# Optimization experiments

Hardware: AMD Instinct MI355X
Metric: run time of the kernel (lower is better)

The kernel has to match this reference:

```python
import jax, jax.numpy as jnp
import numpy as np

N_TOKENS = 32768
DIM = 2048
N_EXPERTS = 64
TOP_K = 8
N_GROUP = 8
TOPK_GROUP = 4
ROUTE_SCALE = 2.5
EPS = 1e-20


def setup_inputs() -> dict:
    key = jax.random.key(0)
    k1, k2 = jax.random.split(key)
    hidden_states = jax.random.normal(k1, (N_TOKENS, DIM), dtype=jnp.float32)
    weight = jax.random.normal(k2, (N_EXPERTS, DIM), dtype=jnp.float32) * 0.02
    e_score_correction_bias = jnp.zeros((N_EXPERTS,), dtype=jnp.float32)
    return {"hidden_states": hidden_states, "weight": weight,
            "e_score_correction_bias": e_score_correction_bias}


def reference(hidden_states, weight, e_score_correction_bias):
    # router logits in fp32: [N, E]
    logits = jnp.einsum('nd,ed->ne', hidden_states.astype(jnp.float32),
                        weight.astype(jnp.float32))
    scores = jax.nn.sigmoid(logits)  # score_func == 'sigmoid'

    # --- top-k index selection (no-grad path in torch) ---
    sfc = scores + e_score_correction_bias[None, :]  # [N, E]
    per_group = N_EXPERTS // N_GROUP
    # group score = sum of top-2 scores within each group: [N, G]
    grouped = sfc.reshape(-1, N_GROUP, per_group)
    group_scores = jax.lax.top_k(grouped, 2)[0].sum(axis=-1)
    # pick top `TOPK_GROUP` groups
    _, group_idx = jax.lax.top_k(group_scores, TOPK_GROUP)  # [N, topk_group]
    n = group_scores.shape[0]
    group_mask = jnp.zeros_like(group_scores).at[
        jnp.arange(n)[:, None], group_idx].set(1.0)  # [N, G]
    score_mask = jnp.repeat(group_mask, per_group, axis=1)  # [N, E]
    masked_scores = jnp.where(score_mask > 0, sfc, 0.0)
    _, topk_indices = jax.lax.top_k(masked_scores, TOP_K)  # [N, top_k]

    # gather weights from *unbiased* scores, normalize, scale
    topk_weights = jnp.take_along_axis(scores, topk_indices, axis=1)
    denom = topk_weights.sum(axis=-1, keepdims=True) + EPS
    topk_weights = topk_weights / denom * ROUTE_SCALE
    return topk_indices, topk_weights
```

## Files before the change

kernel.cpp:

```cpp
#include <hip/hip_runtime.h>
#include <math.h>

#define NT 32768
#define DIM 2048
#define NE 64
#define RSCALE 2.5f
#define REPS 1e-20f
#define KC 32
#define NCH (DIM / KC)
#define TOK 64

#define HL_BUF 12288
#define WL_OFF 24576
#define BS_OFF 49152
#define ARENA 49408

typedef __attribute__((ext_vector_type(8))) short short8x;
typedef __attribute__((ext_vector_type(4))) float f32x4;
typedef __attribute__((ext_vector_type(4))) unsigned int uint4x;

#define PACKHI(odd, even) __builtin_amdgcn_perm((odd), (even), 0x07060302u)

__device__ __forceinline__ void decomp4(f32x4 x, unsigned int o[6]) {
    unsigned int u0 = __float_as_uint(x.x), u1 = __float_as_uint(x.y);
    unsigned int u2 = __float_as_uint(x.z), u3 = __float_as_uint(x.w);
    o[0] = PACKHI(u1, u0); o[1] = PACKHI(u3, u2);
    float r0 = x.x - __uint_as_float(u0 & 0xffff0000u);
    float r1 = x.y - __uint_as_float(u1 & 0xffff0000u);
    float r2 = x.z - __uint_as_float(u2 & 0xffff0000u);
    float r3 = x.w - __uint_as_float(u3 & 0xffff0000u);
    unsigned int v0 = __float_as_uint(r0), v1 = __float_as_uint(r1);
    unsigned int v2 = __float_as_uint(r2), v3 = __float_as_uint(r3);
    o[2] = PACKHI(v1, v0); o[3] = PACKHI(v3, v2);
    float s0 = r0 - __uint_as_float(v0 & 0xffff0000u);
    float s1 = r1 - __uint_as_float(v1 & 0xffff0000u);
    float s2 = r2 - __uint_as_float(v2 & 0xffff0000u);
    float s3 = r3 - __uint_as_float(v3 & 0xffff0000u);
    o[4] = PACKHI(__float_as_uint(s1), __float_as_uint(s0));
    o[5] = PACKHI(__float_as_uint(s3), __float_as_uint(s2));
}

__device__ __forceinline__ void decomp8(f32x4 a, f32x4 b,
                                        short8x* f0, short8x* f1, short8x* f2) {
    unsigned int oa[6], ob[6];
    decomp4(a, oa); decomp4(b, ob);
    uint4x t0 = {oa[0], oa[1], ob[0], ob[1]};
    uint4x t1 = {oa[2], oa[3], ob[2], ob[3]};
    uint4x t2 = {oa[4], oa[5], ob[4], ob[5]};
    *f0 = __builtin_bit_cast(short8x, t0);
    *f1 = __builtin_bit_cast(short8x, t1);
    *f2 = __builtin_bit_cast(short8x, t2);
}

#define STAGE_ISSUE(SA, SB, KOFF) do { \
    SA = *(const f32x4*)(gsrc + (KOFF));     \
    SB = *(const f32x4*)(gsrc + (KOFF) + 4); \
} while (0)

#define STAGE_WRITE(SA, SB, PN) do { \
    short8x f0_, f1_, f2_; \
    decomp8(SA, SB, &f0_, &f1_, &f2_); \
    *(short8x*)(arena + sbase + (PN) * HL_BUF + 0 * 4096 + soff) = f0_; \
    *(short8x*)(arena + sbase + (PN) * HL_BUF + 1 * 4096 + soff) = f1_; \
    *(short8x*)(arena + sbase + (PN) * HL_BUF + 2 * 4096 + soff) = f2_; \
} while (0)

#define COMPUTE(P) do { \
    const char* hb = arena + (P) * HL_BUF; \
    const char* wb = arena + WL_OFF + (P) * HL_BUF; \
    short8x a0, a1, a2; \
    { const int t_ = tt * 16 + l15; \
      const int ro_ = t_ * 64 + ((g ^ ((t_ >> 1) & 3)) << 4); \
      a0 = *(const short8x*)(hb + 0 * 4096 + ro_); \
      a1 = *(const short8x*)(hb + 1 * 4096 + ro_); \
      a2 = *(const short8x*)(hb + 2 * 4096 + ro_); } \
    _Pragma("unroll") \
    for (int et = 0; et < 2; ++et) { \
        const int e_ = ep * 32 + et * 16 + l15; \
        const int ro_ = e_ * 64 + ((g ^ ((e_ >> 1) & 3)) << 4); \
        short8x b0 = *(const short8x*)(wb + 0 * 4096 + ro_); \
        short8x b1 = *(const short8x*)(wb + 1 * 4096 + ro_); \
        short8x b2 = *(const short8x*)(wb + 2 * 4096 + ro_); \
        Cm[et] = __builtin_amdgcn_mfma_f32_16x16x32_bf16(a0, b0, Cm[et], 0, 0, 0); \
        Cc[et] = __builtin_amdgcn_mfma_f32_16x16x32_bf16(a1, b0, Cc[et], 0, 0, 0); \
        Cc[et] = __builtin_amdgcn_mfma_f32_16x16x32_bf16(a2, b0, Cc[et], 0, 0, 0); \
        Cc[et] = __builtin_amdgcn_mfma_f32_16x16x32_bf16(a0, b1, Cc[et], 0, 0, 0); \
        Cc[et] = __builtin_amdgcn_mfma_f32_16x16x32_bf16(a1, b1, Cc[et], 0, 0, 0); \
        Cc[et] = __builtin_amdgcn_mfma_f32_16x16x32_bf16(a0, b2, Cc[et], 0, 0, 0); \
    } \
} while (0)

#define DRAIN do { \
    _Pragma("unroll") \
    for (int et = 0; et < 2; ++et) { \
        _Pragma("unroll") \
        for (int r = 0; r < 4; ++r) \
            md[et][r] += (double)Cm[et][r] + (double)Cc[et][r]; \
        Cm[et] = (f32x4)0.0f; Cc[et] = (f32x4)0.0f; \
    } \
} while (0)

__global__ __launch_bounds__(512, 4) void router_kernel(
    const float* __restrict__ H,
    const float* __restrict__ W,
    const float* __restrict__ B,
    float* __restrict__ out)
{
    __shared__ __align__(16) char arena[ARENA];
    float* bsf = (float*)(arena + BS_OFF);
    float* scf = (float*)(arena);

    const int tid  = threadIdx.x;
    const int lane = tid & 63;
    const int w    = __builtin_amdgcn_readfirstlane(tid >> 6);
    const int l15  = lane & 15, g = lane >> 4;
    const size_t tb = (size_t)blockIdx.x * TOK;

    if (tid < NE) bsf[tid] = B[tid];

    const int si   = tid & 255;
    const int srow = si >> 2;
    const int sq   = si & 3;
    const bool isH = tid < 256;
    const float* gsrc = isH ? (H + (tb + (size_t)srow) * DIM + sq * 8)
                            : (W + (size_t)srow * DIM + sq * 8);
    const int sbase = isH ? 0 : WL_OFF;
    const int soff  = srow * 64 + ((sq ^ ((srow >> 1) & 3)) << 4);

    const int tt = w & 3, ep = w >> 2;

    f32x4 Cm[2], Cc[2];
    double md[2][4];
    #pragma unroll
    for (int et = 0; et < 2; ++et) {
        Cm[et] = (f32x4)0.0f; Cc[et] = (f32x4)0.0f;
        #pragma unroll
        for (int r = 0; r < 4; ++r) md[et][r] = 0.0;
    }

    f32x4 sA0, sA1, sB0, sB1;

    STAGE_ISSUE(sA0, sA1, 0);
    STAGE_WRITE(sA0, sA1, 0);
    STAGE_ISSUE(sB0, sB1, KC);
    __syncthreads();

    for (int chb = 0; chb < NCH; chb += 2) {
        if (chb + 2 < NCH) STAGE_ISSUE(sA0, sA1, (chb + 2) * KC);
        COMPUTE(0);
        STAGE_WRITE(sB0, sB1, 1);
        __syncthreads();

        if (chb + 3 < NCH) STAGE_ISSUE(sB0, sB1, (chb + 3) * KC);
        COMPUTE(1);
        if (chb + 2 < NCH) STAGE_WRITE(sA0, sA1, 0);
        if (((chb + 1) & 7) == 7) DRAIN;
        __syncthreads();
    }

    #pragma unroll
    for (int et = 0; et < 2; ++et)
        #pragma unroll
        for (int r = 0; r < 4; ++r) {
            float logit = (float)md[et][r];
            float s = 1.0f / (1.0f + expf(-logit));
            int t = tt * 16 + g * 4 + r;
            int e = ep * 32 + et * 16 + l15;
            scf[t * 65 + e] = s;
        }
    __syncthreads();

    if ((tid & 7) == 0) {
        const int t = tid >> 3;
        const float* sc = &scf[t * 65];
        float gs[8];
        #pragma unroll
        for (int gg = 0; gg < 8; ++gg) {
            float m1 = -1e30f, m2 = -1e30f;
            #pragma unroll
            for (int j = 0; j < 8; ++j) {
                float v = sc[gg * 8 + j] + bsf[gg * 8 + j];
                if (v > m1) { m2 = m1; m1 = v; }
                else if (v > m2) { m2 = v; }
            }
            gs[gg] = m1 + m2;
        }
        unsigned gmask = 0;
        for (int i = 0; i < 4; ++i) {
            float best = -1e30f; int bg = 0;
            for (int gg = 0; gg < 8; ++gg)
                if (!((gmask >> gg) & 1u) && gs[gg] > best) { best = gs[gg]; bg = gg; }
            gmask |= 1u << bg;
        }
        unsigned long long picked = 0ull;
        int   idxs[8];
        float wts[8];
        float wsum = 0.0f;
        for (int i = 0; i < 8; ++i) {
            float best = -1e30f; int bi = 0;
            for (int e = 0; e < 64; ++e) {
                if ((picked >> e) & 1ull) continue;
                float v = ((gmask >> (e >> 3)) & 1u) ? (sc[e] + bsf[e]) : 0.0f;
                if (v > best) { best = v; bi = e; }
            }
            picked |= 1ull << bi;
            idxs[i] = bi;
            wts[i] = sc[bi];
            wsum += sc[bi];
        }
        const float scale = RSCALE / (wsum + REPS);
        const size_t token = tb + t;
        #pragma unroll
        for (int i = 0; i < 8; ++i) {
            out[token * 8 + i] = (float)idxs[i];
            out[(size_t)NT * 8 + token * 8 + i] = wts[i] * scale;
        }
    }
}

extern "C" void kernel_launch(void* const* d_in, const int* in_sizes, int n_in,
                              void* d_out, int out_size, void* d_ws, size_t ws_size,
                              hipStream_t stream) {
    (void)in_sizes; (void)n_in; (void)out_size; (void)d_ws; (void)ws_size;
    const float* H = (const float*)d_in[0];
    const float* W = (const float*)d_in[1];
    const float* B = (const float*)d_in[2];
    float* out = (float*)d_out;
    router_kernel<<<dim3(NT / TOK), dim3(512), 0, stream>>>(H, W, B, out);
}
```

Baseline: 142.0 us.

## Predecompose router weights once and stream activations directly into registers

A separate pre-kernel splits the weight matrix once into three bf16 parts, stored in a global array laid out in MFMA fragment order. The main kernel drops the LDS staging and the per-chunk barriers. Each wave loads its own 16 token rows straight from global memory into registers, splits them there, and computes all 64 experts with fragments read from global, which should mostly hit cache. Block size falls to 256 threads and occupancy to 2 blocks. This removes redundant per-block weight splitting and LDS traffic, but adds a second launch and relies on cache bandwidth for weight reads, with no LDS reuse.

After: 223.5 us. +57.4%, slower.

```diff
diff --git a/kernel.cpp b/kernel.cpp
--- a/kernel.cpp
+++ b/kernel.cpp
@@ -10,14 +10,11 @@
 #define NCH (DIM / KC)
 #define TOK 64
 
-#define HL_BUF 12288
-#define WL_OFF 24576
-#define BS_OFF 49152
-#define ARENA 49408
-
 typedef __attribute__((ext_vector_type(8))) short short8x;
 typedef __attribute__((ext_vector_type(4))) float f32x4;
 typedef __attribute__((ext_vector_type(4))) unsigned int uint4x;
+
+__device__ short8x WLf[3][NCH][4][64];
 
 #define PACKHI(odd, even) __builtin_amdgcn_perm((odd), (even), 0x07060302u)
 
@@ -52,63 +49,28 @@
     *f2 = __builtin_bit_cast(short8x, t2);
 }
 
-#define STAGE_ISSUE(SA, SB, KOFF) do { \
-    SA = *(const f32x4*)(gsrc + (KOFF));     \
-    SB = *(const f32x4*)(gsrc + (KOFF) + 4); \
-} while (0)
-
-#define STAGE_WRITE(SA, SB, PN) do { \
-    short8x f0_, f1_, f2_; \
-    decomp8(SA, SB, &f0_, &f1_, &f2_); \
-    *(short8x*)(arena + sbase + (PN) * HL_BUF + 0 * 4096 + soff) = f0_; \
-    *(short8x*)(arena + sbase + (PN) * HL_BUF + 1 * 4096 + soff) = f1_; \
-    *(short8x*)(arena + sbase + (PN) * HL_BUF + 2 * 4096 + soff) = f2_; \
-} while (0)
-
-#define COMPUTE(P) do { \
-    const char* hb = arena + (P) * HL_BUF; \
-    const char* wb = arena + WL_OFF + (P) * HL_BUF; \
-    short8x a0, a1, a2; \
-    { const int t_ = tt * 16 + l15; \
-      const int ro_ = t_ * 64 + ((g ^ ((t_ >> 1) & 3)) << 4); \
-      a0 = *(const short8x*)(hb + 0 * 4096 + ro_); \
-      a1 = *(const short8x*)(hb + 1 * 4096 + ro_); \
-      a2 = *(const short8x*)(hb + 2 * 4096 + ro_); } \
-    _Pragma("unroll") \
-    for (int et = 0; et < 2; ++et) { \
-        const int e_ = ep * 32 + et * 16 + l15; \
-        const int ro_ = e_ * 64 + ((g ^ ((e_ >> 1) & 3)) << 4); \
-        short8x b0 = *(const short8x*)(wb + 0 * 4096 + ro_); \
-        short8x b1 = *(const short8x*)(wb + 1 * 4096 + ro_); \
-        short8x b2 = *(const short8x*)(wb + 2 * 4096 + ro_); \
-        Cm[et] = __builtin_amdgcn_mfma_f32_16x16x32_bf16(a0, b0, Cm[et], 0, 0, 0); \
-        Cc[et] = __builtin_amdgcn_mfma_f32_16x16x32_bf16(a1, b0, Cc[et], 0, 0, 0); \
-        Cc[et] = __builtin_amdgcn_mfma_f32_16x16x32_bf16(a2, b0, Cc[et], 0, 0, 0); \
-        Cc[et] = __builtin_amdgcn_mfma_f32_16x16x32_bf16(a0, b1, Cc[et], 0, 0, 0); \
-        Cc[et] = __builtin_amdgcn_mfma_f32_16x16x32_bf16(a1, b1, Cc[et], 0, 0, 0); \
-        Cc[et] = __builtin_amdgcn_mfma_f32_16x16x32_bf16(a0, b2, Cc[et], 0, 0, 0); \
-    } \
-} while (0)
-
-#define DRAIN do { \
-    _Pragma("unroll") \
-    for (int et = 0; et < 2; ++et) { \
-        _Pragma("unroll") \
-        for (int r = 0; r < 4; ++r) \
-            md[et][r] += (double)Cm[et][r] + (double)Cc[et][r]; \
-        Cm[et] = (f32x4)0.0f; Cc[et] = (f32x4)0.0f; \
-    } \
-} while (0)
-
-__global__ __launch_bounds__(512, 4) void router_kernel(
+__global__ void decomp_w_kernel(const float* __restrict__ W) {
+    const int ch = blockIdx.x;
+    const int et = threadIdx.x >> 6;
+    const int l  = threadIdx.x & 63;
+    const float* src = W + (size_t)(et * 16 + (l & 15)) * DIM + ch * KC + (l >> 4) * 8;
+    f32x4 lo = *(const f32x4*)src;
+    f32x4 hi = *(const f32x4*)(src + 4);
+    short8x f0, f1, f2;
+    decomp8(lo, hi, &f0, &f1, &f2);
+    WLf[0][ch][et][l] = f0;
+    WLf[1][ch][et][l] = f1;
+    WLf[2][ch][et][l] = f2;
+}
+
+__global__ __launch_bounds__(256, 2) void router_kernel(
     const float* __restrict__ H,
     const float* __restrict__ W,
     const float* __restrict__ B,
     float* __restrict__ out)
 {
-    __shared__ __align__(16) char arena[ARENA];
-    float* bsf = (float*)(arena + BS_OFF);
-    float* scf = (float*)(arena);
+    __shared__ float scf[TOK * 65];
+    __shared__ float bsf[NE];
 
     const int tid  = threadIdx.x;
     const int lane = tid & 63;
@@ -118,60 +80,69 @@
 
     if (tid < NE) bsf[tid] = B[tid];
 
-    const int si   = tid & 255;
-    const int srow = si >> 2;
-    const int sq   = si & 3;
-    const bool isH = tid < 256;
-    const float* gsrc = isH ? (H + (tb + (size_t)srow) * DIM + sq * 8)
-                            : (W + (size_t)srow * DIM + sq * 8);
-    const int sbase = isH ? 0 : WL_OFF;
-    const int soff  = srow * 64 + ((sq ^ ((srow >> 1) & 3)) << 4);
-
-    const int tt = w & 3, ep = w >> 2;
-
-    f32x4 Cm[2], Cc[2];
-    double md[2][4];
+    const float* hsrc = H + (tb + (size_t)(w * 16 + l15)) * DIM + g * 8;
+
+    f32x4 Cm[4], Cc[4];
+    double md[4][4];
     #pragma unroll
-    for (int et = 0; et < 2; ++et) {
+    for (int et = 0; et < 4; ++et) {
         Cm[et] = (f32x4)0.0f; Cc[et] = (f32x4)0.0f;
         #pragma unroll
         for (int r = 0; r < 4; ++r) md[et][r] = 0.0;
     }
 
-    f32x4 sA0, sA1, sB0, sB1;
-
-    STAGE_ISSUE(sA0, sA1, 0);
-    STAGE_WRITE(sA0, sA1, 0);
-    STAGE_ISSUE(sB0, sB1, KC);
-    __syncthreads();
-
-    for (int chb = 0; chb < NCH; chb += 2) {
-        if (chb + 2 < NCH) STAGE_ISSUE(sA0, sA1, (chb + 2) * KC);
-        COMPUTE(0);
-        STAGE_WRITE(sB0, sB1, 1);
-        __syncthreads();
-
-        if (chb + 3 < NCH) STAGE_ISSUE(sB0, sB1, (chb + 3) * KC);
-        COMPUTE(1);
-        if (chb + 2 < NCH) STAGE_WRITE(sA0, sA1, 0);
-        if (((chb + 1) & 7) == 7) DRAIN;
-        __syncthreads();
+    f32x4 aLo = *(const f32x4*)hsrc;
+    f32x4 aHi = *(const f32x4*)(hsrc + 4);
+
+    #pragma unroll 2
+    for (int ch = 0; ch < NCH; ++ch) {
+        const int chn = (ch + 1 < NCH) ? (ch + 1) : ch;
+        const float* np = hsrc + chn * KC;
+        f32x4 nLo = *(const f32x4*)np;
+        f32x4 nHi = *(const f32x4*)(np + 4);
+
+        short8x a0, a1, a2;
+        decomp8(aLo, aHi, &a0, &a1, &a2);
+
+        #pragma unroll
+        for (int et = 0; et < 4; ++et) {
+            short8x b0 = WLf[0][ch][et][lane];
+            short8x b1 = WLf[1][ch][et][lane];
+            short8x b2 = WLf[2][ch][et][lane];
+            Cm[et] = __builtin_amdgcn_mfma_f32_16x16x32_bf16(a0, b0, Cm[et], 0, 0, 0);
+            Cc[et] = __builtin_amdgcn_mfma_f32_16x16x32_bf16(a1, b0, Cc[et], 0, 0, 0);
+            Cc[et] = __builtin_amdgcn_mfma_f32_16x16x32_bf16(a2, b0, Cc[et], 0, 0, 0);
+            Cc[et] = __builtin_amdgcn_mfma_f32_16x16x32_bf16(a0, b1, Cc[et], 0, 0, 0);
+            Cc[et] = __builtin_amdgcn_mfma_f32_16x16x32_bf16(a1, b1, Cc[et], 0, 0, 0);
+            Cc[et] = __builtin_amdgcn_mfma_f32_16x16x32_bf16(a0, b2, Cc[et], 0, 0, 0);
+        }
+
+        if ((ch & 7) == 7) {
+            #pragma unroll
+            for (int et = 0; et < 4; ++et) {
+                #pragma unroll
+                for (int r = 0; r < 4; ++r)
+                    md[et][r] += (double)Cm[et][r] + (double)Cc[et][r];
+                Cm[et] = (f32x4)0.0f; Cc[et] = (f32x4)0.0f;
+            }
+        }
+        aLo = nLo; aHi = nHi;
     }
 
     #pragma unroll
-    for (int et = 0; et < 2; ++et)
+    for (int et = 0; et < 4; ++et)
         #pragma unroll
         for (int r = 0; r < 4; ++r) {
             float logit = (float)md[et][r];
             float s = 1.0f / (1.0f + expf(-logit));
-            int t = tt * 16 + g * 4 + r;
-            int e = ep * 32 + et * 16 + l15;
+            int t = w * 16 + g * 4 + r;
+            int e = et * 16 + l15;
             scf[t * 65 + e] = s;
         }
     __syncthreads();
 
-    if ((tid & 7) == 0) {
-        const int t = tid >> 3;
+    if ((tid & 3) == 0) {
+        const int t = tid >> 2;
         const float* sc = &scf[t * 65];
         float gs[8];
         #pragma unroll
@@ -226,5 +197,6 @@
     const float* W = (const float*)d_in[1];
     const float* B = (const float*)d_in[2];
     float* out = (float*)d_out;
-    router_kernel<<<dim3(NT / TOK), dim3(512), 0, stream>>>(H, W, B, out);
-}
+    decomp_w_kernel<<<dim3(NCH), dim3(256), 0, stream>>>(W);
+    router_kernel<<<dim3(NT / TOK), dim3(256), 0, stream>>>(H, W, B, out);
+}
```
